# Kernel tuning notes

Hardware: AMD Instinct MI355X
Metric: run time of the kernel (lower is better)

Reference implementation:

```python
import jax, jax.numpy as jnp
import numpy as np

EPS = 1e-5  # torch InstanceNorm1d default eps
H = 64      # band_features


def instance_norm(x):
    # x: [B, T, F]; torch applies InstanceNorm1d on [B, F, T], i.e. normalize
    # over the length axis T per (batch, channel). No affine params.
    mu = jnp.mean(x, axis=1, keepdims=True)
    var = jnp.var(x, axis=1, keepdims=True)  # biased variance, as torch
    return (x - mu) * jax.lax.rsqrt(var + EPS)


def lstm_layer(x, Wih, Whh, bih, bhh):
    # x: [B, T, D_in]; Wih: [4H, D_in]; Whh: [4H, H]; gate order i,f,g,o (torch)
    B, T, _ = x.shape
    xp = jnp.einsum('btd,gd->btg', x, Wih) + bih + bhh   # [B, T, 4H]
    xp = jnp.swapaxes(xp, 0, 1)                          # [T, B, 4H]

    def step(carry, xt):
        h, c = carry
        gates = xt + h @ Whh.T                           # [B, 4H]
        i, f, g, o = jnp.split(gates, 4, axis=-1)
        c = jax.nn.sigmoid(f) * c + jax.nn.sigmoid(i) * jnp.tanh(g)
        h = jax.nn.sigmoid(o) * jnp.tanh(c)
        return (h, c), h

    h0 = jnp.zeros((B, H), x.dtype)
    _, hs = jax.lax.scan(step, (h0, h0), xp)             # hs: [T, B, H]
    return jnp.swapaxes(hs, 0, 1)                        # [B, T, H]


def setup_inputs() -> dict:
    key = jax.random.key(0)
    ks = jax.random.split(key, 12)
    B, T = 64, 4096
    bound = 1.0 / np.sqrt(H)  # torch LSTM/Linear default init scale

    def u(k, shape):
        return jax.random.uniform(k, shape, jnp.float32, -bound, bound)

    return {
        'x': jax.random.normal(ks[0], (B, T, H), jnp.float32),
        'Wih0': u(ks[1], (4 * H, H)), 'Whh0': u(ks[2], (4 * H, H)),
        'bih0': u(ks[3], (4 * H,)),   'bhh0': u(ks[4], (4 * H,)),
        'Wih1': u(ks[5], (4 * H, H)), 'Whh1': u(ks[6], (4 * H, H)),
        'bih1': u(ks[7], (4 * H,)),   'bhh1': u(ks[8], (4 * H,)),
        'Wfc': u(ks[9], (H, H)),      'bfc': u(ks[10], (H,)),
    }


def reference(x, Wih0, Whh0, bih0, bhh0, Wih1, Whh1, bih1, bhh1, Wfc, bfc):
    out = instance_norm(x)
    out = lstm_layer(out, Wih0, Whh0, bih0, bhh0)
    out = lstm_layer(out, Wih1, Whh1, bih1, bhh1)
    out = jnp.einsum('bth,oh->bto', out, Wfc) + bfc
    return out + x
```

## Files before the change

### kernel.cpp

```cpp
#include <hip/hip_runtime.h>
#include <cstddef>
#include <cstdint>

#define BB 64
#define TT 4096
#define HD 64
#define FP 72

typedef _Float16 f16;
typedef _Float16 f16x8 __attribute__((ext_vector_type(8)));
typedef _Float16 f16x4 __attribute__((ext_vector_type(4)));
typedef float f32x4 __attribute__((ext_vector_type(4)));

__device__ __forceinline__ float sigf(float v) {
    return __builtin_amdgcn_rcpf(1.0f + __builtin_amdgcn_exp2f(-1.44269504f * v));
}
__device__ __forceinline__ float tanhf_fast(float v) {
    return 1.0f - 2.0f * __builtin_amdgcn_rcpf(__builtin_amdgcn_exp2f(2.88539008f * v) + 1.0f);
}

__global__ __launch_bounds__(256) void stats_part(const float* __restrict__ x,
                                                  float* __restrict__ part) {
    const int b = blockIdx.x >> 2, seg = blockIdx.x & 3;
    const int f = threadIdx.x & 63, grp = threadIdx.x >> 6;
    const float* xb = x + (size_t)b * TT * HD + (size_t)seg * (TT / 4) * HD;
    float s = 0.f, s2 = 0.f;
    for (int t = grp; t < TT / 4; t += 4) {
        float v = xb[t * HD + f];
        s += v;
        s2 = fmaf(v, v, s2);
    }
    __shared__ float ls[4][64];
    __shared__ float ls2[4][64];
    ls[grp][f] = s;
    ls2[grp][f] = s2;
    __syncthreads();
    if (threadIdx.x < 64) {
        float ss = 0.f, ss2 = 0.f;
#pragma unroll
        for (int i = 0; i < 4; ++i) { ss += ls[i][f]; ss2 += ls2[i][f]; }
        part[blockIdx.x * HD + f] = ss;
        part[256 * HD + blockIdx.x * HD + f] = ss2;
    }
}

__global__ __launch_bounds__(64) void stats_fin(const float* __restrict__ part,
                                                float* __restrict__ stats) {
    const int b = blockIdx.x, f = threadIdx.x;
    float s = 0.f, s2 = 0.f;
#pragma unroll
    for (int seg = 0; seg < 4; ++seg) {
        s += part[(b * 4 + seg) * HD + f];
        s2 += part[256 * HD + (b * 4 + seg) * HD + f];
    }
    float mu = s * (1.0f / TT);
    float var = s2 * (1.0f / TT) - mu * mu;
    stats[b * HD + f] = mu;
    stats[BB * HD + b * HD + f] = rsqrtf(var + 1e-5f);
}

__global__ __launch_bounds__(512, 2) void rnn_mfma(
    const float* __restrict__ x,
    const float* __restrict__ Wih0, const float* __restrict__ Whh0,
    const float* __restrict__ bih0, const float* __restrict__ bhh0,
    const float* __restrict__ Wih1, const float* __restrict__ Whh1,
    const float* __restrict__ bih1, const float* __restrict__ bhh1,
    const float* __restrict__ stats,
    float* __restrict__ h1out) {
    const int blk = blockIdx.x;
    const int tid = threadIdx.x;
    const int lane = tid & 63;
    const int wid = tid >> 6;
    const bool L1w = (wid < 4);
    const int wq = wid & 3;
    const int ln15 = lane & 15;
    const int l16 = lane >> 4;

    __shared__ __align__(16) f16 hT0[2][16 * FP];
    __shared__ __align__(16) f16 hT1[16][16 * FP];
    __shared__ __align__(16) f16 xnb[2][8][16 * FP];

    const float* WA = L1w ? Wih1 : Whh0;
    const float* WBm = L1w ? Whh1 : Wih0;

    uint32_t aA[4][2][4], aB[4][2][4];
#pragma unroll
    for (int i = 0; i < 4; ++i) {
        const int row = 64 * i + 16 * wq + ln15;
#pragma unroll
        for (int kt = 0; kt < 2; ++kt) {
            const int fb = 32 * kt + 8 * l16;
            const float4 a0 = *(const float4*)&WA[row * HD + fb];
            const float4 a1 = *(const float4*)&WA[row * HD + fb + 4];
            const float4 b0 = *(const float4*)&WBm[row * HD + fb];
            const float4 b1 = *(const float4*)&WBm[row * HD + fb + 4];
            f16x8 ha = {(f16)a0.x, (f16)a0.y, (f16)a0.z, (f16)a0.w,
                        (f16)a1.x, (f16)a1.y, (f16)a1.z, (f16)a1.w};
            f16x8 hb = {(f16)b0.x, (f16)b0.y, (f16)b0.z, (f16)b0.w,
                        (f16)b1.x, (f16)b1.y, (f16)b1.z, (f16)b1.w};
            uint4 ua = __builtin_bit_cast(uint4, ha);
            uint4 ub = __builtin_bit_cast(uint4, hb);
            asm volatile("v_accvgpr_write_b32 %0, %1" : "=a"(aA[i][kt][0]) : "v"(ua.x));
            asm volatile("v_accvgpr_write_b32 %0, %1" : "=a"(aA[i][kt][1]) : "v"(ua.y));
            asm volatile("v_accvgpr_write_b32 %0, %1" : "=a"(aA[i][kt][2]) : "v"(ua.z));
            asm volatile("v_accvgpr_write_b32 %0, %1" : "=a"(aA[i][kt][3]) : "v"(ua.w));
            asm volatile("v_accvgpr_write_b32 %0, %1" : "=a"(aB[i][kt][0]) : "v"(ub.x));
            asm volatile("v_accvgpr_write_b32 %0, %1" : "=a"(aB[i][kt][1]) : "v"(ub.y));
            asm volatile("v_accvgpr_write_b32 %0, %1" : "=a"(aB[i][kt][2]) : "v"(ub.z));
            asm volatile("v_accvgpr_write_b32 %0, %1" : "=a"(aB[i][kt][3]) : "v"(ub.w));
        }
    }
    f16x8 wAf[4][2], wBf[4][2];
#pragma unroll
    for (int i = 0; i < 4; ++i)
#pragma unroll
        for (int kt = 0; kt < 2; ++kt) {
            uint4 ua = {aA[i][kt][0], aA[i][kt][1], aA[i][kt][2], aA[i][kt][3]};
            uint4 ub = {aB[i][kt][0], aB[i][kt][1], aB[i][kt][2], aB[i][kt][3]};
            wAf[i][kt] = __builtin_bit_cast(f16x8, ua);
            wBf[i][kt] = __builtin_bit_cast(f16x8, ub);
        }

    const float* bi = L1w ? bih1 : bih0;
    const float* bh = L1w ? bhh1 : bhh0;
    f32x4 bias[4];
#pragma unroll
    for (int i = 0; i < 4; ++i)
#pragma unroll
        for (int r = 0; r < 4; ++r) {
            const int row = 64 * i + 16 * wq + 4 * l16 + r;
            bias[i][r] = bi[row] + bh[row];
        }

    const int sb = tid >> 5;
    const int sq = (tid >> 1) & 15;
    const int sth = tid & 1;
    const size_t gb = (size_t)blk * 16 + sb;
    const float4 mu4 = *(const float4*)&stats[gb * HD + 4 * sq];
    const float4 rs4 = *(const float4*)&stats[(size_t)BB * HD + gb * HD + 4 * sq];
    const float* xrow = x + gb * TT * HD;
    float* orow = h1out + gb * TT * HD;

    for (int i = tid; i < 2 * 16 * FP / 2; i += 512) ((unsigned*)hT0)[i] = 0u;
    for (int i = tid; i < 16 * 16 * FP / 2; i += 512) ((unsigned*)hT1)[i] = 0u;

#pragma unroll
    for (int i = 0; i < 4; ++i) {
        const int tau = sth * 4 + i;
        float4 v = *(const float4*)&xrow[(size_t)tau * HD + 4 * sq];
        f16x4 h4 = {(f16)((v.x - mu4.x) * rs4.x), (f16)((v.y - mu4.y) * rs4.y),
                    (f16)((v.z - mu4.z) * rs4.z), (f16)((v.w - mu4.w) * rs4.w)};
        *(f16x4*)&xnb[0][tau][sb * FP + 4 * sq] = h4;
    }

    float cst[4] = {0.f, 0.f, 0.f, 0.f};

    auto PHASE = [&](int t) {
        const f16* src1 = &hT0[t & 1][0];
        const f16* src2 = L1w ? &hT1[(t + 15) & 15][0]
                              : &xnb[((t + 1) >> 3) & 1][(t + 1) & 7][0];
        f16x8 B1k0 = *(const f16x8*)&src1[ln15 * FP + 8 * l16];
        f16x8 B1k1 = *(const f16x8*)&src1[ln15 * FP + 32 + 8 * l16];
        f16x8 B2k0 = *(const f16x8*)&src2[ln15 * FP + 8 * l16];
        f16x8 B2k1 = *(const f16x8*)&src2[ln15 * FP + 32 + 8 * l16];
        f32x4 acc[4];
#pragma unroll
        for (int i = 0; i < 4; ++i) {
            acc[i] = bias[i];
            acc[i] = __builtin_amdgcn_mfma_f32_16x16x32_f16(wAf[i][0], B1k0, acc[i], 0, 0, 0);
            acc[i] = __builtin_amdgcn_mfma_f32_16x16x32_f16(wAf[i][1], B1k1, acc[i], 0, 0, 0);
            acc[i] = __builtin_amdgcn_mfma_f32_16x16x32_f16(wBf[i][0], B2k0, acc[i], 0, 0, 0);
            acc[i] = __builtin_amdgcn_mfma_f32_16x16x32_f16(wBf[i][1], B2k1, acc[i], 0, 0, 0);
        }
        f16* dest = L1w ? &hT1[t & 15][0] : &hT0[(t + 1) & 1][0];
        f16x4 hv;
#pragma unroll
        for (int r = 0; r < 4; ++r) {
            float ai = sigf(acc[0][r]);
            float af = sigf(acc[1][r]);
            float ag = tanhf_fast(acc[2][r]);
            float ao = sigf(acc[3][r]);
            float c = fmaf(af, cst[r], ai * ag);
            cst[r] = c;
            hv[r] = (f16)(ao * tanhf_fast(c));
        }
        *(f16x4*)&dest[ln15 * FP + 16 * wq + 4 * l16] = hv;
    };

    __syncthreads();
    if (!L1w) PHASE(-1);
    __syncthreads();

    float4 xr[4];
    for (int t = 0; t < TT; ++t) {
        const int tc = t & 7;
        const int cn = (t >> 3) + 1;
        if (tc == 0 && cn < 512) {
#pragma unroll
            for (int i = 0; i < 4; ++i)
                xr[i] = *(const float4*)&xrow[(size_t)(cn * 8 + sth * 4 + i) * HD + 4 * sq];
        }
        PHASE(t);
        if (tc == 3 && t >= 11) {
            const int fch = (t >> 3) - 1;
            const int sbase = (fch & 1) * 8;
#pragma unroll
            for (int i = 0; i < 4; ++i) {
                const int tau = sth * 4 + i;
                f16x4 hvv = *(const f16x4*)&hT1[sbase + tau][sb * FP + 4 * sq];
                float4 o = {(float)hvv[0], (float)hvv[1], (float)hvv[2], (float)hvv[3]};
                *(float4*)&orow[(size_t)(fch * 8 + tau) * HD + 4 * sq] = o;
            }
        }
        if (tc == 5 && cn < 512) {
#pragma unroll
            for (int i = 0; i < 4; ++i) {
                const int tau = sth * 4 + i;
                f16x4 h4 = {(f16)((xr[i].x - mu4.x) * rs4.x), (f16)((xr[i].y - mu4.y) * rs4.y),
                            (f16)((xr[i].z - mu4.z) * rs4.z), (f16)((xr[i].w - mu4.w) * rs4.w)};
                *(f16x4*)&xnb[cn & 1][tau][sb * FP + 4 * sq] = h4;
            }
        }
        __syncthreads();
    }
#pragma unroll
    for (int i = 0; i < 4; ++i) {
        const int tau = sth * 4 + i;
        f16x4 hvv = *(const f16x4*)&hT1[8 + tau][sb * FP + 4 * sq];
        float4 o = {(float)hvv[0], (float)hvv[1], (float)hvv[2], (float)hvv[3]};
        *(float4*)&orow[(size_t)(511 * 8 + tau) * HD + 4 * sq] = o;
    }
}

__global__ __launch_bounds__(256) void fc_res(float* __restrict__ hout,
                                              const float* __restrict__ x,
                                              const float* __restrict__ Wfc,
                                              const float* __restrict__ bfc) {
    __shared__ __align__(16) float wfc_lds[HD * HD];
    __shared__ float bfc_lds[HD];
    const int tid = threadIdx.x;
#pragma unroll
    for (int i = 0; i < 4; ++i)
        ((float4*)wfc_lds)[tid + 256 * i] = ((const float4*)Wfc)[tid + 256 * i];
    if (tid < HD) bfc_lds[tid] = bfc[tid];

    const size_t row = (size_t)blockIdx.x * 256 + tid;
    float hr[HD];
    {
        const float4* hp = (const float4*)(hout + row * HD);
#pragma unroll
        for (int i = 0; i < 16; ++i) {
            float4 v = hp[i];
            hr[4 * i] = v.x; hr[4 * i + 1] = v.y;
            hr[4 * i + 2] = v.z; hr[4 * i + 3] = v.w;
        }
    }
    __syncthreads();

    const float4* xp = (const float4*)(x + row * HD);
    float4* op = (float4*)(hout + row * HD);
    for (int j4 = 0; j4 < 16; ++j4) {
        float s0 = 0.f, s1 = 0.f, s2 = 0.f, s3 = 0.f;
        const float* w0 = &wfc_lds[(4 * j4 + 0) * HD];
        const float* w1 = &wfc_lds[(4 * j4 + 1) * HD];
        const float* w2 = &wfc_lds[(4 * j4 + 2) * HD];
        const float* w3 = &wfc_lds[(4 * j4 + 3) * HD];
#pragma unroll
        for (int k = 0; k < HD; ++k) {
            s0 = fmaf(w0[k], hr[k], s0);
            s1 = fmaf(w1[k], hr[k], s1);
            s2 = fmaf(w2[k], hr[k], s2);
            s3 = fmaf(w3[k], hr[k], s3);
        }
        float4 xv = xp[j4];
        float4 o;
        o.x = s0 + bfc_lds[4 * j4 + 0] + xv.x;
        o.y = s1 + bfc_lds[4 * j4 + 1] + xv.y;
        o.z = s2 + bfc_lds[4 * j4 + 2] + xv.z;
        o.w = s3 + bfc_lds[4 * j4 + 3] + xv.w;
        op[j4] = o;
    }
}

extern "C" void kernel_launch(void* const* d_in, const int* in_sizes, int n_in,
                              void* d_out, int out_size, void* d_ws, size_t ws_size,
                              hipStream_t stream) {
    const float* x    = (const float*)d_in[0];
    const float* Wih0 = (const float*)d_in[1];
    const float* Whh0 = (const float*)d_in[2];
    const float* bih0 = (const float*)d_in[3];
    const float* bhh0 = (const float*)d_in[4];
    const float* Wih1 = (const float*)d_in[5];
    const float* Whh1 = (const float*)d_in[6];
    const float* bih1 = (const float*)d_in[7];
    const float* bhh1 = (const float*)d_in[8];
    const float* Wfc  = (const float*)d_in[9];
    const float* bfc  = (const float*)d_in[10];

    float* part  = (float*)d_ws;
    float* stats = part + 2 * 256 * HD;
    float* out   = (float*)d_out;

    stats_part<<<256, 256, 0, stream>>>(x, part);
    stats_fin<<<64, 64, 0, stream>>>(part, stats);
    rnn_mfma<<<4, 512, 0, stream>>>(x, Wih0, Whh0, bih0, bhh0,
                                    Wih1, Whh1, bih1, bhh1, stats, out);
    fc_res<<<1024, 256, 0, stream>>>(out, x, Wfc, bfc);
}
```

Measured before the change: 3.810 ms.

## Add dedicated I/O warps to RNN kernel and merge gate reciprocals

```diff
diff --git a/kernel.cpp b/kernel.cpp
--- a/kernel.cpp
+++ b/kernel.cpp
@@ -12,11 +12,8 @@
 typedef _Float16 f16x4 __attribute__((ext_vector_type(4)));
 typedef float f32x4 __attribute__((ext_vector_type(4)));
 
-__device__ __forceinline__ float sigf(float v) {
-    return __builtin_amdgcn_rcpf(1.0f + __builtin_amdgcn_exp2f(-1.44269504f * v));
-}
-__device__ __forceinline__ float tanhf_fast(float v) {
-    return 1.0f - 2.0f * __builtin_amdgcn_rcpf(__builtin_amdgcn_exp2f(2.88539008f * v) + 1.0f);
+__device__ __forceinline__ void bar_lgkm() {
+    asm volatile("s_waitcnt lgkmcnt(0)\n\ts_barrier" ::: "memory");
 }
 
 __global__ __launch_bounds__(256) void stats_part(const float* __restrict__ x,
@@ -59,7 +56,7 @@
     stats[BB * HD + b * HD + f] = rsqrtf(var + 1e-5f);
 }
 
-__global__ __launch_bounds__(512, 2) void rnn_mfma(
+__global__ __launch_bounds__(768, 2) void rnn_mfma(
     const float* __restrict__ x,
     const float* __restrict__ Wih0, const float* __restrict__ Whh0,
     const float* __restrict__ bih0, const float* __restrict__ bhh0,
@@ -71,6 +68,7 @@
     const int tid = threadIdx.x;
     const int lane = tid & 63;
     const int wid = tid >> 6;
+    const bool isCompute = (wid < 8);
     const bool L1w = (wid < 4);
     const int wq = wid & 3;
     const int ln15 = lane & 15;
@@ -80,77 +78,83 @@
     __shared__ __align__(16) f16 hT1[16][16 * FP];
     __shared__ __align__(16) f16 xnb[2][8][16 * FP];
 
-    const float* WA = L1w ? Wih1 : Whh0;
-    const float* WBm = L1w ? Whh1 : Wih0;
-
-    uint32_t aA[4][2][4], aB[4][2][4];
-#pragma unroll
-    for (int i = 0; i < 4; ++i) {
-        const int row = 64 * i + 16 * wq + ln15;
-#pragma unroll
-        for (int kt = 0; kt < 2; ++kt) {
-            const int fb = 32 * kt + 8 * l16;
-            const float4 a0 = *(const float4*)&WA[row * HD + fb];
-            const float4 a1 = *(const float4*)&WA[row * HD + fb + 4];
-            const float4 b0 = *(const float4*)&WBm[row * HD + fb];
-            const float4 b1 = *(const float4*)&WBm[row * HD + fb + 4];
-            f16x8 ha = {(f16)a0.x, (f16)a0.y, (f16)a0.z, (f16)a0.w,
-                        (f16)a1.x, (f16)a1.y, (f16)a1.z, (f16)a1.w};
-            f16x8 hb = {(f16)b0.x, (f16)b0.y, (f16)b0.z, (f16)b0.w,
-                        (f16)b1.x, (f16)b1.y, (f16)b1.z, (f16)b1.w};
-            uint4 ua = __builtin_bit_cast(uint4, ha);
-            uint4 ub = __builtin_bit_cast(uint4, hb);
-            asm volatile("v_accvgpr_write_b32 %0, %1" : "=a"(aA[i][kt][0]) : "v"(ua.x));
-            asm volatile("v_accvgpr_write_b32 %0, %1" : "=a"(aA[i][kt][1]) : "v"(ua.y));
-            asm volatile("v_accvgpr_write_b32 %0, %1" : "=a"(aA[i][kt][2]) : "v"(ua.z));
-            asm volatile("v_accvgpr_write_b32 %0, %1" : "=a"(aA[i][kt][3]) : "v"(ua.w));
-            asm volatile("v_accvgpr_write_b32 %0, %1" : "=a"(aB[i][kt][0]) : "v"(ub.x));
-            asm volatile("v_accvgpr_write_b32 %0, %1" : "=a"(aB[i][kt][1]) : "v"(ub.y));
-            asm volatile("v_accvgpr_write_b32 %0, %1" : "=a"(aB[i][kt][2]) : "v"(ub.z));
-            asm volatile("v_accvgpr_write_b32 %0, %1" : "=a"(aB[i][kt][3]) : "v"(ub.w));
-        }
-    }
     f16x8 wAf[4][2], wBf[4][2];
-#pragma unroll
-    for (int i = 0; i < 4; ++i)
-#pragma unroll
-        for (int kt = 0; kt < 2; ++kt) {
-            uint4 ua = {aA[i][kt][0], aA[i][kt][1], aA[i][kt][2], aA[i][kt][3]};
-            uint4 ub = {aB[i][kt][0], aB[i][kt][1], aB[i][kt][2], aB[i][kt][3]};
-            wAf[i][kt] = __builtin_bit_cast(f16x8, ua);
-            wBf[i][kt] = __builtin_bit_cast(f16x8, ub);
-        }
-
-    const float* bi = L1w ? bih1 : bih0;
-    const float* bh = L1w ? bhh1 : bhh0;
     f32x4 bias[4];
-#pragma unroll
-    for (int i = 0; i < 4; ++i)
-#pragma unroll
-        for (int r = 0; r < 4; ++r) {
-            const int row = 64 * i + 16 * wq + 4 * l16 + r;
-            bias[i][r] = bi[row] + bh[row];
-        }
-
-    const int sb = tid >> 5;
-    const int sq = (tid >> 1) & 15;
-    const int sth = tid & 1;
-    const size_t gb = (size_t)blk * 16 + sb;
-    const float4 mu4 = *(const float4*)&stats[gb * HD + 4 * sq];
-    const float4 rs4 = *(const float4*)&stats[(size_t)BB * HD + gb * HD + 4 * sq];
-    const float* xrow = x + gb * TT * HD;
-    float* orow = h1out + gb * TT * HD;
-
-    for (int i = tid; i < 2 * 16 * FP / 2; i += 512) ((unsigned*)hT0)[i] = 0u;
-    for (int i = tid; i < 16 * 16 * FP / 2; i += 512) ((unsigned*)hT1)[i] = 0u;
-
-#pragma unroll
-    for (int i = 0; i < 4; ++i) {
-        const int tau = sth * 4 + i;
-        float4 v = *(const float4*)&xrow[(size_t)tau * HD + 4 * sq];
-        f16x4 h4 = {(f16)((v.x - mu4.x) * rs4.x), (f16)((v.y - mu4.y) * rs4.y),
-                    (f16)((v.z - mu4.z) * rs4.z), (f16)((v.w - mu4.w) * rs4.w)};
-        *(f16x4*)&xnb[0][tau][sb * FP + 4 * sq] = h4;
+    if (isCompute) {
+        const float* WA = L1w ? Wih1 : Whh0;
+        const float* WBm = L1w ? Whh1 : Wih0;
+        uint32_t aA[4][2][4], aB[4][2][4];
+#pragma unroll
+        for (int i = 0; i < 4; ++i) {
+            const int row = 64 * i + 16 * wq + ln15;
+#pragma unroll
+            for (int kt = 0; kt < 2; ++kt) {
+                const int fb = 32 * kt + 8 * l16;
+                const float4 a0 = *(const float4*)&WA[row * HD + fb];
+                const float4 a1 = *(const float4*)&WA[row * HD + fb + 4];
+                const float4 b0 = *(const float4*)&WBm[row * HD + fb];
+                const float4 b1 = *(const float4*)&WBm[row * HD + fb + 4];
+                f16x8 ha = {(f16)a0.x, (f16)a0.y, (f16)a0.z, (f16)a0.w,
+                            (f16)a1.x, (f16)a1.y, (f16)a1.z, (f16)a1.w};
+                f16x8 hb = {(f16)b0.x, (f16)b0.y, (f16)b0.z, (f16)b0.w,
+                            (f16)b1.x, (f16)b1.y, (f16)b1.z, (f16)b1.w};
+                uint4 ua = __builtin_bit_cast(uint4, ha);
+                uint4 ub = __builtin_bit_cast(uint4, hb);
+                asm volatile("v_accvgpr_write_b32 %0, %1" : "=a"(aA[i][kt][0]) : "v"(ua.x));
+                asm volatile("v_accvgpr_write_b32 %0, %1" : "=a"(aA[i][kt][1]) : "v"(ua.y));
+                asm volatile("v_accvgpr_write_b32 %0, %1" : "=a"(aA[i][kt][2]) : "v"(ua.z));
+                asm volatile("v_accvgpr_write_b32 %0, %1" : "=a"(aA[i][kt][3]) : "v"(ua.w));
+                asm volatile("v_accvgpr_write_b32 %0, %1" : "=a"(aB[i][kt][0]) : "v"(ub.x));
+                asm volatile("v_accvgpr_write_b32 %0, %1" : "=a"(aB[i][kt][1]) : "v"(ub.y));
+                asm volatile("v_accvgpr_write_b32 %0, %1" : "=a"(aB[i][kt][2]) : "v"(ub.z));
+                asm volatile("v_accvgpr_write_b32 %0, %1" : "=a"(aB[i][kt][3]) : "v"(ub.w));
+            }
+        }
+#pragma unroll
+        for (int i = 0; i < 4; ++i)
+#pragma unroll
+            for (int kt = 0; kt < 2; ++kt) {
+                uint4 ua = {aA[i][kt][0], aA[i][kt][1], aA[i][kt][2], aA[i][kt][3]};
+                uint4 ub = {aB[i][kt][0], aB[i][kt][1], aB[i][kt][2], aB[i][kt][3]};
+                wAf[i][kt] = __builtin_bit_cast(f16x8, ua);
+                wBf[i][kt] = __builtin_bit_cast(f16x8, ub);
+            }
+        const float* bi = L1w ? bih1 : bih0;
+        const float* bh = L1w ? bhh1 : bhh0;
+#pragma unroll
+        for (int i = 0; i < 4; ++i)
+#pragma unroll
+            for (int r = 0; r < 4; ++r) {
+                const int row = 64 * i + 16 * wq + 4 * l16 + r;
+                bias[i][r] = bi[row] + bh[row];
+            }
+    }
+
+    const int stid = tid - 512;
+    const int sb = stid >> 4;
+    const int sq = stid & 15;
+    float4 mu4 = {0, 0, 0, 0}, rs4 = {0, 0, 0, 0};
+    const float* xrow = nullptr;
+    float* orow = nullptr;
+    if (!isCompute) {
+        const size_t gb = (size_t)blk * 16 + sb;
+        mu4 = *(const float4*)&stats[gb * HD + 4 * sq];
+        rs4 = *(const float4*)&stats[(size_t)BB * HD + gb * HD + 4 * sq];
+        xrow = x + gb * TT * HD;
+        orow = h1out + gb * TT * HD;
+    }
+
+    for (int i = tid; i < 2 * 16 * FP / 2; i += 768) ((unsigned*)hT0)[i] = 0u;
+    for (int i = tid; i < 16 * 16 * FP / 2; i += 768) ((unsigned*)hT1)[i] = 0u;
+
+    if (!isCompute) {
+#pragma unroll
+        for (int tau = 0; tau < 8; ++tau) {
+            float4 v = *(const float4*)&xrow[(size_t)tau * HD + 4 * sq];
+            f16x4 h4 = {(f16)((v.x - mu4.x) * rs4.x), (f16)((v.y - mu4.y) * rs4.y),
+                        (f16)((v.z - mu4.z) * rs4.z), (f16)((v.w - mu4.w) * rs4.w)};
+            *(f16x4*)&xnb[0][tau][sb * FP + 4 * sq] = h4;
+        }
     }
 
     float cst[4] = {0.f, 0.f, 0.f, 0.f};
@@ -176,59 +180,68 @@
         f16x4 hv;
 #pragma unroll
         for (int r = 0; r < 4; ++r) {
-            float ai = sigf(acc[0][r]);
-            float af = sigf(acc[1][r]);
-            float ag = tanhf_fast(acc[2][r]);
-            float ao = sigf(acc[3][r]);
-            float c = fmaf(af, cst[r], ai * ag);
+            float emi = __builtin_amdgcn_exp2f(-1.44269504f * acc[0][r]);
+            float emf = __builtin_amdgcn_exp2f(-1.44269504f * acc[1][r]);
+            float eg2 = __builtin_amdgcn_exp2f(2.88539008f * acc[2][r]);
+            float emo = __builtin_amdgcn_exp2f(-1.44269504f * acc[3][r]);
+            float ig = (eg2 - 1.0f) *
+                       __builtin_amdgcn_rcpf((1.0f + emi) * (eg2 + 1.0f));
+            float fg = __builtin_amdgcn_rcpf(1.0f + emf);
+            float c = fmaf(fg, cst[r], ig);
             cst[r] = c;
-            hv[r] = (f16)(ao * tanhf_fast(c));
+            float ec2 = __builtin_amdgcn_exp2f(2.88539008f * c);
+            hv[r] = (f16)((ec2 - 1.0f) *
+                          __builtin_amdgcn_rcpf((1.0f + emo) * (ec2 + 1.0f)));
         }
         *(f16x4*)&dest[ln15 * FP + 16 * wq + 4 * l16] = hv;
     };
 
-    __syncthreads();
-    if (!L1w) PHASE(-1);
-    __syncthreads();
-
-    float4 xr[4];
+    bar_lgkm();
+    if (isCompute && !L1w) PHASE(-1);
+    bar_lgkm();
+
+    float4 xr[8];
     for (int t = 0; t < TT; ++t) {
-        const int tc = t & 7;
-        const int cn = (t >> 3) + 1;
-        if (tc == 0 && cn < 512) {
-#pragma unroll
-            for (int i = 0; i < 4; ++i)
-                xr[i] = *(const float4*)&xrow[(size_t)(cn * 8 + sth * 4 + i) * HD + 4 * sq];
-        }
-        PHASE(t);
-        if (tc == 3 && t >= 11) {
-            const int fch = (t >> 3) - 1;
-            const int sbase = (fch & 1) * 8;
-#pragma unroll
-            for (int i = 0; i < 4; ++i) {
-                const int tau = sth * 4 + i;
-                f16x4 hvv = *(const f16x4*)&hT1[sbase + tau][sb * FP + 4 * sq];
-                float4 o = {(float)hvv[0], (float)hvv[1], (float)hvv[2], (float)hvv[3]};
-                *(float4*)&orow[(size_t)(fch * 8 + tau) * HD + 4 * sq] = o;
-            }
-        }
-        if (tc == 5 && cn < 512) {
-#pragma unroll
-            for (int i = 0; i < 4; ++i) {
-                const int tau = sth * 4 + i;
-                f16x4 h4 = {(f16)((xr[i].x - mu4.x) * rs4.x), (f16)((xr[i].y - mu4.y) * rs4.y),
-                            (f16)((xr[i].z - mu4.z) * rs4.z), (f16)((xr[i].w - mu4.w) * rs4.w)};
-                *(f16x4*)&xnb[cn & 1][tau][sb * FP + 4 * sq] = h4;
-            }
-        }
-        __syncthreads();
-    }
-#pragma unroll
-    for (int i = 0; i < 4; ++i) {
-        const int tau = sth * 4 + i;
-        f16x4 hvv = *(const f16x4*)&hT1[8 + tau][sb * FP + 4 * sq];
-        float4 o = {(float)hvv[0], (float)hvv[1], (float)hvv[2], (float)hvv[3]};
-        *(float4*)&orow[(size_t)(511 * 8 + tau) * HD + 4 * sq] = o;
+        if (isCompute) {
+            PHASE(t);
+        } else {
+            const int tc = t & 7;
+            const int cn = (t >> 3) + 1;
+            if (tc == 0 && cn < 512) {
+#pragma unroll
+                for (int tau = 0; tau < 8; ++tau)
+                    xr[tau] = *(const float4*)&xrow[(size_t)(cn * 8 + tau) * HD + 4 * sq];
+            }
+            if (tc == 2 && t >= 10) {
+                const int fch = (t >> 3) - 1;
+                const int sbase = (fch & 1) * 8;
+#pragma unroll
+                for (int tau = 0; tau < 8; ++tau) {
+                    f16x4 hvv = *(const f16x4*)&hT1[sbase + tau][sb * FP + 4 * sq];
+                    float4 o = {(float)hvv[0], (float)hvv[1], (float)hvv[2], (float)hvv[3]};
+                    *(float4*)&orow[(size_t)(fch * 8 + tau) * HD + 4 * sq] = o;
+                }
+            }
+            if (tc == 5 && cn < 512) {
+#pragma unroll
+                for (int tau = 0; tau < 8; ++tau) {
+                    f16x4 h4 = {(f16)((xr[tau].x - mu4.x) * rs4.x),
+                                (f16)((xr[tau].y - mu4.y) * rs4.y),
+                                (f16)((xr[tau].z - mu4.z) * rs4.z),
+                                (f16)((xr[tau].w - mu4.w) * rs4.w)};
+                    *(f16x4*)&xnb[cn & 1][tau][sb * FP + 4 * sq] = h4;
+                }
+            }
+        }
+        bar_lgkm();
+    }
+    if (!isCompute) {
+#pragma unroll
+        for (int tau = 0; tau < 8; ++tau) {
+            f16x4 hvv = *(const f16x4*)&hT1[8 + tau][sb * FP + 4 * sq];
+            float4 o = {(float)hvv[0], (float)hvv[1], (float)hvv[2], (float)hvv[3]};
+            *(float4*)&orow[(size_t)(511 * 8 + tau) * HD + 4 * sq] = o;
+        }
     }
 }
 
@@ -303,7 +316,7 @@
 
     stats_part<<<256, 256, 0, stream>>>(x, part);
     stats_fin<<<64, 64, 0, stream>>>(part, stats);
-    rnn_mfma<<<4, 512, 0, stream>>>(x, Wih0, Whh0, bih0, bhh0,
+    rnn_mfma<<<4, 768, 0, stream>>>(x, Wih0, Whh0, bih0, bhh0,
                                     Wih1, Whh1, bih1, bhh1, stats, out);
     fc_res<<<1024, 256, 0, stream>>>(out, x, Wfc, bfc);
 }
```

After: 4.876 ms. +28.0%, slower.

## Unroll recurrence by 16, spread x/out I/O per step, merge gate reciprocals

Applied to the files above, without the earlier changes.

```diff
diff --git a/kernel.cpp b/kernel.cpp
--- a/kernel.cpp
+++ b/kernel.cpp
@@ -10,13 +10,12 @@
 typedef _Float16 f16;
 typedef _Float16 f16x8 __attribute__((ext_vector_type(8)));
 typedef _Float16 f16x4 __attribute__((ext_vector_type(4)));
+typedef _Float16 f16x2 __attribute__((ext_vector_type(2)));
 typedef float f32x4 __attribute__((ext_vector_type(4)));
-
-__device__ __forceinline__ float sigf(float v) {
-    return __builtin_amdgcn_rcpf(1.0f + __builtin_amdgcn_exp2f(-1.44269504f * v));
-}
-__device__ __forceinline__ float tanhf_fast(float v) {
-    return 1.0f - 2.0f * __builtin_amdgcn_rcpf(__builtin_amdgcn_exp2f(2.88539008f * v) + 1.0f);
+typedef float v2f __attribute__((ext_vector_type(2)));
+
+__device__ __forceinline__ void bar_lgkm() {
+    asm volatile("s_waitcnt lgkmcnt(0)\n\ts_barrier" ::: "memory");
 }
 
 __global__ __launch_bounds__(256) void stats_part(const float* __restrict__ x,
@@ -82,7 +81,6 @@
 
     const float* WA = L1w ? Wih1 : Whh0;
     const float* WBm = L1w ? Whh1 : Wih0;
-
     uint32_t aA[4][2][4], aB[4][2][4];
 #pragma unroll
     for (int i = 0; i < 4; ++i) {
@@ -133,32 +131,36 @@
         }
 
     const int sb = tid >> 5;
-    const int sq = (tid >> 1) & 15;
-    const int sth = tid & 1;
+    const int f2 = (tid & 31) * 2;
     const size_t gb = (size_t)blk * 16 + sb;
-    const float4 mu4 = *(const float4*)&stats[gb * HD + 4 * sq];
-    const float4 rs4 = *(const float4*)&stats[(size_t)BB * HD + gb * HD + 4 * sq];
+    const float mux = stats[gb * HD + f2];
+    const float muy = stats[gb * HD + f2 + 1];
+    const float rsx = stats[(size_t)BB * HD + gb * HD + f2];
+    const float rsy = stats[(size_t)BB * HD + gb * HD + f2 + 1];
+    const v2f aa = {rsx, rsy};
+    const v2f bbv = {-mux * rsx, -muy * rsy};
     const float* xrow = x + gb * TT * HD;
     float* orow = h1out + gb * TT * HD;
 
     for (int i = tid; i < 2 * 16 * FP / 2; i += 512) ((unsigned*)hT0)[i] = 0u;
     for (int i = tid; i < 16 * 16 * FP / 2; i += 512) ((unsigned*)hT1)[i] = 0u;
 
-#pragma unroll
-    for (int i = 0; i < 4; ++i) {
-        const int tau = sth * 4 + i;
-        float4 v = *(const float4*)&xrow[(size_t)tau * HD + 4 * sq];
-        f16x4 h4 = {(f16)((v.x - mu4.x) * rs4.x), (f16)((v.y - mu4.y) * rs4.y),
-                    (f16)((v.z - mu4.z) * rs4.z), (f16)((v.w - mu4.w) * rs4.w)};
-        *(f16x4*)&xnb[0][tau][sb * FP + 4 * sq] = h4;
-    }
-
-    float cst[4] = {0.f, 0.f, 0.f, 0.f};
-
-    auto PHASE = [&](int t) {
-        const f16* src1 = &hT0[t & 1][0];
-        const f16* src2 = L1w ? &hT1[(t + 15) & 15][0]
-                              : &xnb[((t + 1) >> 3) & 1][(t + 1) & 7][0];
+    v2f xr[8];
+#pragma unroll
+    for (int tau = 0; tau < 8; ++tau) {
+        v2f v = *(const v2f*)&xrow[(size_t)tau * HD + f2];
+        f16x2 xh;
+        xh.x = (f16)fmaf(v.x, aa.x, bbv.x);
+        xh.y = (f16)fmaf(v.y, aa.y, bbv.y);
+        *(f16x2*)&xnb[0][tau][sb * FP + f2] = xh;
+    }
+#pragma unroll
+    for (int tau = 0; tau < 8; ++tau)
+        xr[tau] = *(const v2f*)&xrow[(size_t)(8 + tau) * HD + f2];
+
+    v2f cstp[2] = {{0.f, 0.f}, {0.f, 0.f}};
+
+    auto PHASE = [&](const f16* src1, const f16* src2, f16* dest) {
         f16x8 B1k0 = *(const f16x8*)&src1[ln15 * FP + 8 * l16];
         f16x8 B1k1 = *(const f16x8*)&src1[ln15 * FP + 32 + 8 * l16];
         f16x8 B2k0 = *(const f16x8*)&src2[ln15 * FP + 8 * l16];
@@ -172,63 +174,85 @@
             acc[i] = __builtin_amdgcn_mfma_f32_16x16x32_f16(wBf[i][0], B2k0, acc[i], 0, 0, 0);
             acc[i] = __builtin_amdgcn_mfma_f32_16x16x32_f16(wBf[i][1], B2k1, acc[i], 0, 0, 0);
         }
-        f16* dest = L1w ? &hT1[t & 15][0] : &hT0[(t + 1) & 1][0];
-        f16x4 hv;
-#pragma unroll
-        for (int r = 0; r < 4; ++r) {
-            float ai = sigf(acc[0][r]);
-            float af = sigf(acc[1][r]);
-            float ag = tanhf_fast(acc[2][r]);
-            float ao = sigf(acc[3][r]);
-            float c = fmaf(af, cst[r], ai * ag);
-            cst[r] = c;
-            hv[r] = (f16)(ao * tanhf_fast(c));
-        }
-        *(f16x4*)&dest[ln15 * FP + 16 * wq + 4 * l16] = hv;
+        uint32_t hw[2];
+#pragma unroll
+        for (int rp = 0; rp < 2; ++rp) {
+            v2f gi = {acc[0][2 * rp], acc[0][2 * rp + 1]};
+            v2f gf = {acc[1][2 * rp], acc[1][2 * rp + 1]};
+            v2f gg = {acc[2][2 * rp], acc[2][2 * rp + 1]};
+            v2f go = {acc[3][2 * rp], acc[3][2 * rp + 1]};
+            v2f ti = gi * -1.44269504f;
+            v2f tf = gf * -1.44269504f;
+            v2f tg = gg * 2.88539008f;
+            v2f to = go * -1.44269504f;
+            v2f emi = {__builtin_amdgcn_exp2f(ti.x), __builtin_amdgcn_exp2f(ti.y)};
+            v2f emf = {__builtin_amdgcn_exp2f(tf.x), __builtin_amdgcn_exp2f(tf.y)};
+            v2f eg2 = {__builtin_amdgcn_exp2f(tg.x), __builtin_amdgcn_exp2f(tg.y)};
+            v2f emo = {__builtin_amdgcn_exp2f(to.x), __builtin_amdgcn_exp2f(to.y)};
+            v2f dig = (emi + 1.0f) * (eg2 + 1.0f);
+            v2f rig = {__builtin_amdgcn_rcpf(dig.x), __builtin_amdgcn_rcpf(dig.y)};
+            v2f ig = (eg2 - 1.0f) * rig;
+            v2f dnf = emf + 1.0f;
+            v2f fg2 = {__builtin_amdgcn_rcpf(dnf.x), __builtin_amdgcn_rcpf(dnf.y)};
+            v2f c = fg2 * cstp[rp] + ig;
+            cstp[rp] = c;
+            v2f tc2 = c * 2.88539008f;
+            v2f ec2 = {__builtin_amdgcn_exp2f(tc2.x), __builtin_amdgcn_exp2f(tc2.y)};
+            v2f dno = (emo + 1.0f) * (ec2 + 1.0f);
+            v2f rno = {__builtin_amdgcn_rcpf(dno.x), __builtin_amdgcn_rcpf(dno.y)};
+            v2f h = (ec2 - 1.0f) * rno;
+            f16x2 hh;
+            hh.x = (f16)h.x;
+            hh.y = (f16)h.y;
+            hw[rp] = __builtin_bit_cast(uint32_t, hh);
+        }
+        uint2 hu = {hw[0], hw[1]};
+        *(f16x4*)&dest[ln15 * FP + 16 * wq + 4 * l16] = __builtin_bit_cast(f16x4, hu);
     };
 
-    __syncthreads();
-    if (!L1w) PHASE(-1);
-    __syncthreads();
-
-    float4 xr[4];
-    for (int t = 0; t < TT; ++t) {
-        const int tc = t & 7;
-        const int cn = (t >> 3) + 1;
-        if (tc == 0 && cn < 512) {
-#pragma unroll
-            for (int i = 0; i < 4; ++i)
-                xr[i] = *(const float4*)&xrow[(size_t)(cn * 8 + sth * 4 + i) * HD + 4 * sq];
-        }
-        PHASE(t);
-        if (tc == 3 && t >= 11) {
-            const int fch = (t >> 3) - 1;
-            const int sbase = (fch & 1) * 8;
-#pragma unroll
-            for (int i = 0; i < 4; ++i) {
-                const int tau = sth * 4 + i;
-                f16x4 hvv = *(const f16x4*)&hT1[sbase + tau][sb * FP + 4 * sq];
-                float4 o = {(float)hvv[0], (float)hvv[1], (float)hvv[2], (float)hvv[3]};
-                *(float4*)&orow[(size_t)(fch * 8 + tau) * HD + 4 * sq] = o;
+    bar_lgkm();
+    if (!L1w) PHASE(&hT0[1][0], &xnb[0][0][0], &hT0[0][0]);
+    bar_lgkm();
+
+    for (int tb = 0; tb < TT; tb += 16) {
+#pragma unroll
+        for (int k = 0; k < 16; ++k) {
+            {
+                const f16* src1 = &hT0[k & 1][0];
+                const f16* src2 = L1w ? &hT1[(k + 15) & 15][0]
+                                      : &xnb[((k + 1) >> 3) & 1][(k + 1) & 7][0];
+                f16* dest = L1w ? &hT1[k & 15][0] : &hT0[(k + 1) & 1][0];
+                PHASE(src1, src2, dest);
             }
-        }
-        if (tc == 5 && cn < 512) {
-#pragma unroll
-            for (int i = 0; i < 4; ++i) {
-                const int tau = sth * 4 + i;
-                f16x4 h4 = {(f16)((xr[i].x - mu4.x) * rs4.x), (f16)((xr[i].y - mu4.y) * rs4.y),
-                            (f16)((xr[i].z - mu4.z) * rs4.z), (f16)((xr[i].w - mu4.w) * rs4.w)};
-                *(f16x4*)&xnb[cn & 1][tau][sb * FP + 4 * sq] = h4;
+            if (tb > 0 || k >= 2) {
+                f16x2 hh = *(const f16x2*)&hT1[(k + 14) & 15][sb * FP + f2];
+                v2f o = {(float)hh.x, (float)hh.y};
+                *(v2f*)&orow[(size_t)(tb + k - 2) * HD + f2] = o;
             }
-        }
-        __syncthreads();
-    }
-#pragma unroll
-    for (int i = 0; i < 4; ++i) {
-        const int tau = sth * 4 + i;
-        f16x4 hvv = *(const f16x4*)&hT1[8 + tau][sb * FP + 4 * sq];
-        float4 o = {(float)hvv[0], (float)hvv[1], (float)hvv[2], (float)hvv[3]};
-        *(float4*)&orow[(size_t)(511 * 8 + tau) * HD + 4 * sq] = o;
+            {
+                const int tc = k & 7;
+                if (k < 8 || tb < TT - 16) {
+                    const int bufw = (k < 8) ? 1 : 0;
+                    v2f v = xr[tc];
+                    f16x2 xh;
+                    xh.x = (f16)fmaf(v.x, aa.x, bbv.x);
+                    xh.y = (f16)fmaf(v.y, aa.y, bbv.y);
+                    *(f16x2*)&xnb[bufw][tc][sb * FP + f2] = xh;
+                }
+                if (tb < TT - 16) {
+                    xr[tc] = *(const v2f*)&xrow[(size_t)(tb + 16 + k) * HD + f2];
+                }
+            }
+            bar_lgkm();
+        }
+    }
+    {
+        f16x2 h14 = *(const f16x2*)&hT1[14][sb * FP + f2];
+        v2f o14 = {(float)h14.x, (float)h14.y};
+        *(v2f*)&orow[(size_t)(TT - 2) * HD + f2] = o14;
+        f16x2 h15 = *(const f16x2*)&hT1[15][sb * FP + f2];
+        v2f o15 = {(float)h15.x, (float)h15.y};
+        *(v2f*)&orow[(size_t)(TT - 1) * HD + f2] = o15;
     }
 }
 
```

Result: faster. 3.296 ms (-13.5%).
